# Kernel tuning notes

Measured on AMD Instinct MI355X. Metric: run time of the kernel, lower is better.

The kernel has to match this reference:

```python
import jax, jax.numpy as jnp
import numpy as np
import math

D_MODEL = 512
N_HEADS = 8
D_FF = 2048
EPS = 1e-5

def _layernorm(x, g, b):
    m = jnp.mean(x, axis=-1, keepdims=True)
    v = jnp.var(x, axis=-1, keepdims=True)
    return (x - m) * jax.lax.rsqrt(v + EPS) * g + b

def setup_inputs() -> dict:
    key = jax.random.key(0)
    ks = jax.random.split(key, 8)
    d, dff = D_MODEL, D_FF
    s = lambda fan: 1.0 / math.sqrt(fan)
    return {
        "x": jax.random.normal(ks[0], (4, 2048, d), dtype=jnp.float32),
        "w_qkv": jax.random.normal(ks[1], (d, 3 * d), dtype=jnp.float32) * s(d),
        "b_qkv": jnp.zeros((3 * d,), dtype=jnp.float32),
        "w1": jax.random.normal(ks[2], (d, dff), dtype=jnp.float32) * s(d),
        "b1": jnp.zeros((dff,), dtype=jnp.float32),
        "w2": jax.random.normal(ks[3], (dff, d), dtype=jnp.float32) * s(dff),
        "b2": jnp.zeros((d,), dtype=jnp.float32),
        "g1": jnp.ones((d,), dtype=jnp.float32),
        "be1": jnp.zeros((d,), dtype=jnp.float32),
        "g2": jnp.ones((d,), dtype=jnp.float32),
        "be2": jnp.zeros((d,), dtype=jnp.float32),
    }

def reference(x, w_qkv, b_qkv, w1, b1, w2, b2, g1, be1, g2, be2):
    B, L, d = x.shape
    H = N_HEADS
    hd = d // H
    # Faithful to original: scale = 1/sqrt(hd), scores = qk / scale = qk * sqrt(hd)
    inv_scale = math.sqrt(hd)
    qkv = x @ w_qkv + b_qkv            # [B, L, 3d]
    q, k, v = jnp.split(qkv, 3, axis=-1)
    split_heads = lambda t: t.reshape(B, L, H, hd).transpose(0, 2, 1, 3)  # [B,H,L,hd]
    q, k, v = map(split_heads, (q, k, v))
    scores = jnp.einsum('bhqd,bhkd->bhqk', q, k) * inv_scale
    attn = jax.nn.softmax(scores, axis=-1)
    out = jnp.einsum('bhqk,bhkd->bhqd', attn, v)
    out = out.transpose(0, 2, 1, 3).reshape(B, L, d)
    x = _layernorm(x + out, g1, be1)
    ff = jax.nn.relu(x @ w1 + b1) @ w2 + b2
    return _layernorm(x + ff, g2, be2)
```

## Files before the change

### kernel.cpp

```cpp
#include <hip/hip_runtime.h>

typedef _Float16 f16;
typedef _Float16 f16x4 __attribute__((ext_vector_type(4)));
typedef _Float16 f16x8 __attribute__((ext_vector_type(8)));
typedef float    f32x4 __attribute__((ext_vector_type(4)));

#define QK_SCALE 11.5416528f

__device__ __forceinline__ void g2l16(const void* g, void* l) {
  __builtin_amdgcn_global_load_lds(
      (__attribute__((address_space(1))) const unsigned int*)g,
      (__attribute__((address_space(3))) unsigned int*)l, 16, 0, 0);
}

__device__ __forceinline__ f32x4 mfma16(f16x8 a, f16x8 b, f32x4 c) {
  return __builtin_amdgcn_mfma_f32_16x16x32_f16(a, b, c, 0, 0, 0);
}

__device__ __forceinline__ int swz64(int row, int c) { return row * 64 + ((c ^ (row & 7)) << 3); }
__device__ __forceinline__ int swz32(int row, int c) { return row * 32 + ((c ^ ((row >> 1) & 3)) << 3); }

__global__ __launch_bounds__(256) void k_split(const float* __restrict__ in,
                                               f16* __restrict__ hi, f16* __restrict__ lo, int n4) {
  int i = blockIdx.x * 256 + threadIdx.x;
  if (i >= n4) return;
  f32x4 v = ((const f32x4*)in)[i];
  f16x4 h, l;
#pragma unroll
  for (int j = 0; j < 4; ++j) {
    f16 hv = (f16)v[j];
    h[j] = hv;
    l[j] = (f16)(v[j] - (float)hv);
  }
  ((f16x4*)hi)[i] = h;
  ((f16x4*)lo)[i] = l;
}

template <bool WLO>
__global__ __launch_bounds__(256) void k_transpose_split(const float* __restrict__ in, int K, int N,
                                                         f16* __restrict__ oh, f16* __restrict__ ol) {
  __shared__ float t[32][33];
  const int tx = threadIdx.x, ty = threadIdx.y;
  const int n0 = blockIdx.x * 32, k0 = blockIdx.y * 32;
#pragma unroll
  for (int j = 0; j < 4; ++j)
    t[ty + j * 8][tx] = in[(size_t)(k0 + ty + j * 8) * N + n0 + tx];
  __syncthreads();
#pragma unroll
  for (int j = 0; j < 4; ++j) {
    float v = t[tx][ty + j * 8];
    f16 hv = (f16)v;
    size_t o = (size_t)(n0 + ty + j * 8) * K + k0 + tx;
    oh[o] = hv;
    if (WLO) ol[o] = (f16)(v - (float)hv);
  }
}

template <int EPI, bool SPLIT>
__global__ __launch_bounds__(256, SPLIT ? 2 : 3) void k_gemm(
    const f16* __restrict__ Ah, const f16* __restrict__ Al,
    const f16* __restrict__ Bh, const f16* __restrict__ Bl,
    const float* __restrict__ bias,
    float* __restrict__ outF, f16* __restrict__ outH,
    f16* __restrict__ oqh, f16* __restrict__ oql,
    f16* __restrict__ okh, f16* __restrict__ ovT,
    int M, int N, int K) {
  constexpr int NB = SPLIT ? 2 : 1;
  __shared__ f16 As[NB][128 * 32];
  __shared__ f16 Bs[NB][128 * 32];

  const int tid = threadIdx.x;
  const int bm = blockIdx.x, bn = blockIdx.y;
  const int w = tid >> 6, lane = tid & 63;
  const int wr = w >> 1, wc = w & 1;
  const int lrow = lane & 15, lgrp = lane >> 4;

  f32x4 acc[4][4] = {};

  const int nkt = K >> 5;
  for (int kt = 0; kt < nkt; ++kt) {
    __syncthreads();
    const int kk = kt << 5;
#pragma unroll
    for (int c = 0; c < 2; ++c) {
      const int i = tid + (c << 8);
      const int row = i >> 2;
      const int gch = ((i & 3) ^ ((i >> 3) & 3)) << 3;
      const size_t aoff = (size_t)(bm * 128 + row) * K + kk + gch;
      const size_t boff = (size_t)(bn * 128 + row) * K + kk + gch;
      g2l16(Ah + aoff, &As[0][i * 8]);
      g2l16(Bh + boff, &Bs[0][i * 8]);
      if (SPLIT) {
        g2l16(Al + aoff, &As[1][i * 8]);
        g2l16(Bl + boff, &Bs[1][i * 8]);
      }
    }
    __syncthreads();

    f16x8 a0[4], a1[4], b0[4], b1[4];
#pragma unroll
    for (int mf = 0; mf < 4; ++mf) {
      const int off = swz32(wr * 64 + mf * 16 + lrow, lgrp);
      a0[mf] = *(const f16x8*)&As[0][off];
      if (SPLIT) a1[mf] = *(const f16x8*)&As[SPLIT ? 1 : 0][off];
    }
#pragma unroll
    for (int nf = 0; nf < 4; ++nf) {
      const int off = swz32(wc * 64 + nf * 16 + lrow, lgrp);
      b0[nf] = *(const f16x8*)&Bs[0][off];
      if (SPLIT) b1[nf] = *(const f16x8*)&Bs[SPLIT ? 1 : 0][off];
    }
#pragma unroll
    for (int mf = 0; mf < 4; ++mf)
#pragma unroll
      for (int nf = 0; nf < 4; ++nf) {
        acc[mf][nf] = mfma16(a0[mf], b0[nf], acc[mf][nf]);
        if (SPLIT) {
          acc[mf][nf] = mfma16(a0[mf], b1[nf], acc[mf][nf]);
          acc[mf][nf] = mfma16(a1[mf], b0[nf], acc[mf][nf]);
        }
      }
  }

  const int rowbase = bm * 128 + wr * 64 + lgrp * 4;
  const int colbase = bn * 128 + wc * 64 + lrow;
#pragma unroll
  for (int mf = 0; mf < 4; ++mf) {
#pragma unroll
    for (int nf = 0; nf < 4; ++nf) {
      const int gc = colbase + nf * 16;
      const float bv = bias[gc];
#pragma unroll
      for (int r = 0; r < 4; ++r) {
        const int gr = rowbase + mf * 16 + r;
        const float val = acc[mf][nf][r] + bv;
        if (EPI == 0) {
          const int bb = gr >> 11, tok = gr & 2047;
          const int kind = gc >> 9, hh = (gc >> 6) & 7, dd = gc & 63;
          const size_t bhp = (size_t)((bb << 3) + hh);
          const size_t qidx = (bhp * 2048 + tok) * 64 + dd;
          if (kind == 0) {
            const float sv = val * QK_SCALE;
            const f16 hv = (f16)sv;
            oqh[qidx] = hv; oql[qidx] = (f16)(sv - (float)hv);
          } else if (kind == 1) {
            okh[qidx] = (f16)val;
          } else {
            ovT[(bhp * 64 + dd) * 2048 + tok] = (f16)val;
          }
        } else if (EPI == 1) {
          outH[(size_t)gr * N + gc] = (f16)fmaxf(val, 0.f);
        } else {
          outF[(size_t)gr * N + gc] = val;
        }
      }
    }
  }
}

__global__ __launch_bounds__(256, 3) void k_attn(
    const f16* __restrict__ Qh, const f16* __restrict__ Ql,
    const f16* __restrict__ Kh, const f16* __restrict__ Vt,
    float* __restrict__ out) {
  __shared__ f16 sKh[2][64 * 64], sVt[2][64 * 64];
  __shared__ f16 sPt[4][16 * 64];

  const int tid = threadIdx.x;
  const int qt = blockIdx.x, bh = blockIdx.y;
  const int w = tid >> 6, lane = tid & 63;
  const int lrow = lane & 15, lgrp = lane >> 4;

  const size_t qbase = (((size_t)bh * 2048) + qt * 64 + w * 16) * 64;
  f16x8 qh8[2], ql8[2];
#pragma unroll
  for (int ks = 0; ks < 2; ++ks) {
    const size_t o = qbase + (size_t)lrow * 64 + (ks * 4 + lgrp) * 8;
    qh8[ks] = *(const f16x8*)(Qh + o);
    ql8[ks] = *(const f16x8*)(Ql + o);
  }

  float m_run = -3e38f;
  float l_run = 0.f;
  f32x4 oacc[4] = {};

  auto stage = [&](int b, int kt) {
    const size_t koff = ((size_t)bh * 2048 + (size_t)kt * 64) * 64;
    const size_t voff = (size_t)bh * 64 * 2048 + (size_t)kt * 64;
#pragma unroll
    for (int c = 0; c < 2; ++c) {
      const int i = tid + (c << 8);
      const int row = i >> 3;
      const int gch = ((i & 7) ^ (row & 7)) << 3;
      g2l16(Kh + koff + (size_t)row * 64 + gch, &sKh[b][i * 8]);
      g2l16(Vt + voff + (size_t)row * 2048 + gch, &sVt[b][i * 8]);
    }
  };

  stage(0, 0);
  __syncthreads();

  for (int kt = 0; kt < 32; ++kt) {
    const int cur = kt & 1;
    if (kt < 31) stage(cur ^ 1, kt + 1);

    f32x4 sacc[4] = {};
    __builtin_amdgcn_s_setprio(1);
#pragma unroll
    for (int ks = 0; ks < 2; ++ks) {
#pragma unroll
      for (int kf = 0; kf < 4; ++kf) {
        const int off = swz64(kf * 16 + lrow, ks * 4 + lgrp);
        const f16x8 kh8 = *(const f16x8*)&sKh[cur][off];
        sacc[kf] = mfma16(kh8, qh8[ks], sacc[kf]);
        sacc[kf] = mfma16(kh8, ql8[ks], sacc[kf]);
      }
    }
    __builtin_amdgcn_s_setprio(0);

    {
      float mt = sacc[0][0];
#pragma unroll
      for (int kf = 0; kf < 4; ++kf)
#pragma unroll
        for (int r = 0; r < 4; ++r) mt = fmaxf(mt, sacc[kf][r]);
      mt = fmaxf(mt, __shfl_xor(mt, 16, 64));
      mt = fmaxf(mt, __shfl_xor(mt, 32, 64));
      float mcur = m_run;
      if (!__all(mt <= mcur + 8.0f)) {
        const float mnew = fmaxf(mcur, mt);
        const float corr = __builtin_amdgcn_exp2f(mcur - mnew);
        m_run = mnew;
        l_run *= corr;
#pragma unroll
        for (int hf = 0; hf < 4; ++hf) oacc[hf] = oacc[hf] * corr;
        mcur = mnew;
      }
      float ps = 0.f;
#pragma unroll
      for (int kf = 0; kf < 4; ++kf) {
        f16x4 pv;
#pragma unroll
        for (int r = 0; r < 4; ++r) {
          const float p = __builtin_amdgcn_exp2f(sacc[kf][r] - mcur);
          ps += p;
          pv[r] = (f16)p;
        }
        *(f16x4*)&sPt[w][swz64(lrow, kf * 2 + (lgrp >> 1)) + ((lgrp & 1) << 2)] = pv;
      }
      ps += __shfl_xor(ps, 16, 64);
      ps += __shfl_xor(ps, 32, 64);
      l_run += ps;
    }

    __builtin_amdgcn_s_setprio(1);
#pragma unroll
    for (int ks = 0; ks < 2; ++ks) {
      const f16x8 pb = *(const f16x8*)&sPt[w][swz64(lrow, ks * 4 + lgrp)];
#pragma unroll
      for (int hf = 0; hf < 4; ++hf) {
        const f16x8 va = *(const f16x8*)&sVt[cur][swz64(hf * 16 + lrow, ks * 4 + lgrp)];
        oacc[hf] = mfma16(va, pb, oacc[hf]);
      }
    }
    __builtin_amdgcn_s_setprio(0);
    __syncthreads();
  }

  const int b = bh >> 3, h = bh & 7;
  const float inv = 1.0f / l_run;
  const int t = b * 2048 + qt * 64 + w * 16 + lrow;
#pragma unroll
  for (int hf = 0; hf < 4; ++hf) {
    f32x4 o = oacc[hf] * inv;
    *(f32x4*)(out + (size_t)t * 512 + h * 64 + hf * 16 + lgrp * 4) = o;
  }
}

__global__ __launch_bounds__(64) void k_ln(const float* __restrict__ X, const float* __restrict__ R,
                                           const float* __restrict__ g, const float* __restrict__ be,
                                           float* __restrict__ outF, f16* __restrict__ outH) {
  const int row = blockIdx.x, t = threadIdx.x;
  const size_t base = (size_t)row * 512 + t * 8;
  f32x4 x0 = *(const f32x4*)(X + base);
  f32x4 x1 = *(const f32x4*)(X + base + 4);
  f32x4 r0 = *(const f32x4*)(R + base);
  f32x4 r1 = *(const f32x4*)(R + base + 4);
  x0 = x0 + r0;
  x1 = x1 + r1;
  float s = 0.f, ss = 0.f;
#pragma unroll
  for (int j = 0; j < 4; ++j) { s += x0[j] + x1[j]; ss += x0[j] * x0[j] + x1[j] * x1[j]; }
#pragma unroll
  for (int o = 32; o; o >>= 1) {
    s += __shfl_xor(s, o, 64);
    ss += __shfl_xor(ss, o, 64);
  }
  const float mean = s * (1.f / 512.f);
  const float var = ss * (1.f / 512.f) - mean * mean;
  const float rs = rsqrtf(var + 1e-5f);
  f32x4 g0 = *(const f32x4*)(g + t * 8);
  f32x4 g1v = *(const f32x4*)(g + t * 8 + 4);
  f32x4 b0 = *(const f32x4*)(be + t * 8);
  f32x4 b1 = *(const f32x4*)(be + t * 8 + 4);
  f32x4 y0 = (x0 - mean) * rs * g0 + b0;
  f32x4 y1 = (x1 - mean) * rs * g1v + b1;
  *(f32x4*)(outF + base) = y0;
  *(f32x4*)(outF + base + 4) = y1;
  if (outH != nullptr) {
    f16x8 hx;
#pragma unroll
    for (int j = 0; j < 4; ++j) { hx[j] = (f16)y0[j]; hx[j + 4] = (f16)y1[j]; }
    *(f16x8*)(outH + base) = hx;
  }
}

extern "C" void kernel_launch(void* const* d_in, const int* in_sizes, int n_in,
                              void* d_out, int out_size, void* d_ws, size_t ws_size,
                              hipStream_t stream) {
  (void)in_sizes; (void)n_in; (void)out_size;
  const float* x = (const float*)d_in[0];
  const float* w_qkv = (const float*)d_in[1];
  const float* b_qkv = (const float*)d_in[2];
  const float* w1 = (const float*)d_in[3];
  const float* b1 = (const float*)d_in[4];
  const float* w2 = (const float*)d_in[5];
  const float* b2 = (const float*)d_in[6];
  const float* g1 = (const float*)d_in[7];
  const float* be1 = (const float*)d_in[8];
  const float* g2 = (const float*)d_in[9];
  const float* be2 = (const float*)d_in[10];
  float* out = (float*)d_out;

  char* p = (char*)d_ws;
  auto take = [&](size_t bytes) {
    char* r = p;
    p += (bytes + 255) & ~(size_t)255;
    return r;
  };
  f16* xh = (f16*)take(8192ull * 512 * 2);
  f16* xl = (f16*)take(8192ull * 512 * 2);
  f16* wqkvTh = (f16*)take(1536ull * 512 * 2);
  f16* wqkvTl = (f16*)take(1536ull * 512 * 2);
  f16* w1T = (f16*)take(2048ull * 512 * 2);
  f16* w2T = (f16*)take(512ull * 2048 * 2);
  f16* qh = (f16*)take(32ull * 2048 * 64 * 2);
  f16* ql = (f16*)take(32ull * 2048 * 64 * 2);
  f16* kh = (f16*)take(32ull * 2048 * 64 * 2);
  f16* vT = (f16*)take(32ull * 64 * 2048 * 2);
  float* attn = (float*)take(8192ull * 512 * 4);
  float* x1f = (float*)take(8192ull * 512 * 4);
  f16* x1h = (f16*)take(8192ull * 512 * 2);
  f16* hbuf = qh;
  float* ffb = attn;

  if ((size_t)(p - (char*)d_ws) > ws_size) return;

  dim3 tb(32, 8);
  k_split<<<4096, 256, 0, stream>>>(x, xh, xl, 8192 * 512 / 4);
  k_transpose_split<true><<<dim3(1536 / 32, 512 / 32), tb, 0, stream>>>(w_qkv, 512, 1536, wqkvTh, wqkvTl);
  k_transpose_split<false><<<dim3(2048 / 32, 512 / 32), tb, 0, stream>>>(w1, 512, 2048, w1T, nullptr);
  k_transpose_split<false><<<dim3(512 / 32, 2048 / 32), tb, 0, stream>>>(w2, 2048, 512, w2T, nullptr);

  k_gemm<0, true><<<dim3(64, 12), 256, 0, stream>>>(xh, xl, wqkvTh, wqkvTl, b_qkv,
                                                    nullptr, nullptr, qh, ql, kh, vT,
                                                    8192, 1536, 512);
  k_attn<<<dim3(32, 32), 256, 0, stream>>>(qh, ql, kh, vT, attn);
  k_ln<<<8192, 64, 0, stream>>>(x, attn, g1, be1, x1f, x1h);
  k_gemm<1, false><<<dim3(64, 16), 256, 0, stream>>>(x1h, nullptr, w1T, nullptr, b1,
                                                     nullptr, hbuf, nullptr, nullptr, nullptr, nullptr,
                                                     8192, 2048, 512);
  k_gemm<2, false><<<dim3(64, 4), 256, 0, stream>>>(hbuf, nullptr, w2T, nullptr, b2,
                                                    ffb, nullptr, nullptr, nullptr, nullptr, nullptr,
                                                    8192, 512, 2048);
  k_ln<<<8192, 64, 0, stream>>>(x1f, ffb, g2, be2, out, nullptr);
}
```

Measured before the change: 213.2 us.

## Use 32x32 MFMA in attention with register-resident P and skip lo-split for V

The attention kernel switches from 16x16x32 to 32x32x16 MFMA tiles, with each wave handling 32 query rows and each block 128 rows. The softmax probabilities are packed with cvt_pkrtz and rearranged in registers with permlane32 swaps, so the shared-memory round trip for P is gone. Separately, the QKV GEMM skips the low-part split products for the V columns (bn >= 8), cutting MFMA work and loads there at some cost in V precision. Occupancy drops from 3 to 2 blocks per CU, and there are half as many attention blocks.

```diff
diff --git a/kernel.cpp b/kernel.cpp
--- a/kernel.cpp
+++ b/kernel.cpp
@@ -4,6 +4,8 @@
 typedef _Float16 f16x4 __attribute__((ext_vector_type(4)));
 typedef _Float16 f16x8 __attribute__((ext_vector_type(8)));
 typedef float    f32x4 __attribute__((ext_vector_type(4)));
+typedef float    f32x16 __attribute__((ext_vector_type(16)));
+typedef unsigned int u32x4 __attribute__((ext_vector_type(4)));
 
 #define QK_SCALE 11.5416528f
 
@@ -15,6 +17,16 @@
 
 __device__ __forceinline__ f32x4 mfma16(f16x8 a, f16x8 b, f32x4 c) {
   return __builtin_amdgcn_mfma_f32_16x16x32_f16(a, b, c, 0, 0, 0);
+}
+__device__ __forceinline__ f32x16 mfma32(f16x8 a, f16x8 b, f32x16 c) {
+  return __builtin_amdgcn_mfma_f32_32x32x16_f16(a, b, c, 0, 0, 0);
+}
+__device__ __forceinline__ unsigned pkrtz(float a, float b) {
+  auto t = __builtin_amdgcn_cvt_pkrtz(a, b);
+  return *(unsigned*)&t;
+}
+__device__ __forceinline__ void swap32(unsigned& a, unsigned& b) {
+  asm volatile("v_permlane32_swap_b32 %0, %1" : "+v"(a), "+v"(b));
 }
 
 __device__ __forceinline__ int swz64(int row, int c) { return row * 64 + ((c ^ (row & 7)) << 3); }
@@ -75,6 +87,8 @@
   const int wr = w >> 1, wc = w & 1;
   const int lrow = lane & 15, lgrp = lane >> 4;
 
+  const bool useLo = SPLIT && !(EPI == 0 && bn >= 8);
+
   f32x4 acc[4][4] = {};
 
   const int nkt = K >> 5;
@@ -90,10 +104,11 @@
       const size_t boff = (size_t)(bn * 128 + row) * K + kk + gch;
       g2l16(Ah + aoff, &As[0][i * 8]);
       g2l16(Bh + boff, &Bs[0][i * 8]);
-      if (SPLIT) {
-        g2l16(Al + aoff, &As[1][i * 8]);
-        g2l16(Bl + boff, &Bs[1][i * 8]);
-      }
+      if (SPLIT)
+        if (useLo) {
+          g2l16(Al + aoff, &As[1][i * 8]);
+          g2l16(Bl + boff, &Bs[1][i * 8]);
+        }
     }
     __syncthreads();
 
@@ -102,23 +117,26 @@
     for (int mf = 0; mf < 4; ++mf) {
       const int off = swz32(wr * 64 + mf * 16 + lrow, lgrp);
       a0[mf] = *(const f16x8*)&As[0][off];
-      if (SPLIT) a1[mf] = *(const f16x8*)&As[SPLIT ? 1 : 0][off];
+      if (SPLIT)
+        if (useLo) a1[mf] = *(const f16x8*)&As[SPLIT ? 1 : 0][off];
     }
 #pragma unroll
     for (int nf = 0; nf < 4; ++nf) {
       const int off = swz32(wc * 64 + nf * 16 + lrow, lgrp);
       b0[nf] = *(const f16x8*)&Bs[0][off];
-      if (SPLIT) b1[nf] = *(const f16x8*)&Bs[SPLIT ? 1 : 0][off];
+      if (SPLIT)
+        if (useLo) b1[nf] = *(const f16x8*)&Bs[SPLIT ? 1 : 0][off];
     }
 #pragma unroll
     for (int mf = 0; mf < 4; ++mf)
 #pragma unroll
       for (int nf = 0; nf < 4; ++nf) {
         acc[mf][nf] = mfma16(a0[mf], b0[nf], acc[mf][nf]);
-        if (SPLIT) {
-          acc[mf][nf] = mfma16(a0[mf], b1[nf], acc[mf][nf]);
-          acc[mf][nf] = mfma16(a1[mf], b0[nf], acc[mf][nf]);
-        }
+        if (SPLIT)
+          if (useLo) {
+            acc[mf][nf] = mfma16(a0[mf], b1[nf], acc[mf][nf]);
+            acc[mf][nf] = mfma16(a1[mf], b0[nf], acc[mf][nf]);
+          }
       }
   }
 
@@ -158,30 +176,26 @@
   }
 }
 
-__global__ __launch_bounds__(256, 3) void k_attn(
+__global__ __launch_bounds__(256, 2) void k_attn(
     const f16* __restrict__ Qh, const f16* __restrict__ Ql,
     const f16* __restrict__ Kh, const f16* __restrict__ Vt,
     float* __restrict__ out) {
-  __shared__ f16 sKh[2][64 * 64], sVt[2][64 * 64];
-  __shared__ f16 sPt[4][16 * 64];
+  __shared__ f16 sK[2][64 * 64], sV[2][64 * 64];
 
   const int tid = threadIdx.x;
   const int qt = blockIdx.x, bh = blockIdx.y;
   const int w = tid >> 6, lane = tid & 63;
-  const int lrow = lane & 15, lgrp = lane >> 4;
-
-  const size_t qbase = (((size_t)bh * 2048) + qt * 64 + w * 16) * 64;
-  f16x8 qh8[2], ql8[2];
-#pragma unroll
-  for (int ks = 0; ks < 2; ++ks) {
-    const size_t o = qbase + (size_t)lrow * 64 + (ks * 4 + lgrp) * 8;
-    qh8[ks] = *(const f16x8*)(Qh + o);
-    ql8[ks] = *(const f16x8*)(Ql + o);
-  }
-
-  float m_run = -3e38f;
-  float l_run = 0.f;
-  f32x4 oacc[4] = {};
+  const int lh = lane & 31, hh = lane >> 5;
+
+  const int qrow = qt * 128 + w * 32 + lh;
+  const size_t qoff = ((size_t)bh * 2048 + qrow) * 64;
+  f16x8 qh8[4], ql8[4];
+#pragma unroll
+  for (int d = 0; d < 4; ++d) {
+    const size_t o = qoff + d * 16 + hh * 8;
+    qh8[d] = *(const f16x8*)(Qh + o);
+    ql8[d] = *(const f16x8*)(Ql + o);
+  }
 
   auto stage = [&](int b, int kt) {
     const size_t koff = ((size_t)bh * 2048 + (size_t)kt * 64) * 64;
@@ -191,10 +205,14 @@
       const int i = tid + (c << 8);
       const int row = i >> 3;
       const int gch = ((i & 7) ^ (row & 7)) << 3;
-      g2l16(Kh + koff + (size_t)row * 64 + gch, &sKh[b][i * 8]);
-      g2l16(Vt + voff + (size_t)row * 2048 + gch, &sVt[b][i * 8]);
+      g2l16(Kh + koff + (size_t)row * 64 + gch, &sK[b][i * 8]);
+      g2l16(Vt + voff + (size_t)row * 2048 + gch, &sV[b][i * 8]);
     }
   };
+
+  float m_run = -3e38f;
+  float l_run = 0.f;
+  f32x16 oacc[2] = {};
 
   stage(0, 0);
   __syncthreads();
@@ -203,77 +221,86 @@
     const int cur = kt & 1;
     if (kt < 31) stage(cur ^ 1, kt + 1);
 
-    f32x4 sacc[4] = {};
+    f32x16 s[2] = {};
     __builtin_amdgcn_s_setprio(1);
 #pragma unroll
-    for (int ks = 0; ks < 2; ++ks) {
-#pragma unroll
-      for (int kf = 0; kf < 4; ++kf) {
-        const int off = swz64(kf * 16 + lrow, ks * 4 + lgrp);
-        const f16x8 kh8 = *(const f16x8*)&sKh[cur][off];
-        sacc[kf] = mfma16(kh8, qh8[ks], sacc[kf]);
-        sacc[kf] = mfma16(kh8, ql8[ks], sacc[kf]);
-      }
+    for (int d = 0; d < 4; ++d) {
+      const f16x8 k0 = *(const f16x8*)&sK[cur][swz64(lh, d * 2 + hh)];
+      const f16x8 k1 = *(const f16x8*)&sK[cur][swz64(32 + lh, d * 2 + hh)];
+      s[0] = mfma32(k0, qh8[d], s[0]);
+      s[0] = mfma32(k0, ql8[d], s[0]);
+      s[1] = mfma32(k1, qh8[d], s[1]);
+      s[1] = mfma32(k1, ql8[d], s[1]);
     }
     __builtin_amdgcn_s_setprio(0);
 
-    {
-      float mt = sacc[0][0];
-#pragma unroll
-      for (int kf = 0; kf < 4; ++kf)
-#pragma unroll
-        for (int r = 0; r < 4; ++r) mt = fmaxf(mt, sacc[kf][r]);
-      mt = fmaxf(mt, __shfl_xor(mt, 16, 64));
-      mt = fmaxf(mt, __shfl_xor(mt, 32, 64));
-      float mcur = m_run;
-      if (!__all(mt <= mcur + 8.0f)) {
-        const float mnew = fmaxf(mcur, mt);
-        const float corr = __builtin_amdgcn_exp2f(mcur - mnew);
-        m_run = mnew;
-        l_run *= corr;
-#pragma unroll
-        for (int hf = 0; hf < 4; ++hf) oacc[hf] = oacc[hf] * corr;
-        mcur = mnew;
-      }
-      float ps = 0.f;
-#pragma unroll
-      for (int kf = 0; kf < 4; ++kf) {
-        f16x4 pv;
-#pragma unroll
-        for (int r = 0; r < 4; ++r) {
-          const float p = __builtin_amdgcn_exp2f(sacc[kf][r] - mcur);
-          ps += p;
-          pv[r] = (f16)p;
-        }
-        *(f16x4*)&sPt[w][swz64(lrow, kf * 2 + (lgrp >> 1)) + ((lgrp & 1) << 2)] = pv;
-      }
-      ps += __shfl_xor(ps, 16, 64);
-      ps += __shfl_xor(ps, 32, 64);
-      l_run += ps;
-    }
+    float mt = s[0][0];
+#pragma unroll
+    for (int r = 0; r < 16; ++r) { mt = fmaxf(mt, s[0][r]); mt = fmaxf(mt, s[1][r]); }
+    mt = fmaxf(mt, __shfl_xor(mt, 32, 64));
+    float mcur = m_run;
+    if (!__all(mt <= mcur + 8.0f)) {
+      const float mnew = fmaxf(mcur, mt);
+      const float corr = __builtin_amdgcn_exp2f(mcur - mnew);
+      m_run = mnew;
+      l_run *= corr;
+      oacc[0] = oacc[0] * corr;
+      oacc[1] = oacc[1] * corr;
+      mcur = mnew;
+    }
+    float ps = 0.f;
+    unsigned pk0[8], pk1[8];
+#pragma unroll
+    for (int i = 0; i < 8; ++i) {
+      const float a0 = __builtin_amdgcn_exp2f(s[0][2 * i] - mcur);
+      const float a1 = __builtin_amdgcn_exp2f(s[0][2 * i + 1] - mcur);
+      const float b0 = __builtin_amdgcn_exp2f(s[1][2 * i] - mcur);
+      const float b1 = __builtin_amdgcn_exp2f(s[1][2 * i + 1] - mcur);
+      ps += (a0 + a1) + (b0 + b1);
+      pk0[i] = pkrtz(a0, a1);
+      pk1[i] = pkrtz(b0, b1);
+    }
+    ps += __shfl_xor(ps, 32, 64);
+    l_run += ps;
+
+    swap32(pk0[0], pk0[2]); swap32(pk0[1], pk0[3]);
+    swap32(pk0[4], pk0[6]); swap32(pk0[5], pk0[7]);
+    swap32(pk1[0], pk1[2]); swap32(pk1[1], pk1[3]);
+    swap32(pk1[4], pk1[6]); swap32(pk1[5], pk1[7]);
+
+    u32x4 pbu[4];
+    pbu[0] = (u32x4){pk0[0], pk0[1], pk0[2], pk0[3]};
+    pbu[1] = (u32x4){pk0[4], pk0[5], pk0[6], pk0[7]};
+    pbu[2] = (u32x4){pk1[0], pk1[1], pk1[2], pk1[3]};
+    pbu[3] = (u32x4){pk1[4], pk1[5], pk1[6], pk1[7]};
 
     __builtin_amdgcn_s_setprio(1);
 #pragma unroll
-    for (int ks = 0; ks < 2; ++ks) {
-      const f16x8 pb = *(const f16x8*)&sPt[w][swz64(lrow, ks * 4 + lgrp)];
-#pragma unroll
-      for (int hf = 0; hf < 4; ++hf) {
-        const f16x8 va = *(const f16x8*)&sVt[cur][swz64(hf * 16 + lrow, ks * 4 + lgrp)];
-        oacc[hf] = mfma16(va, pb, oacc[hf]);
+    for (int s2 = 0; s2 < 4; ++s2) {
+      const f16x8 pb = *(const f16x8*)&pbu[s2];
+#pragma unroll
+      for (int db = 0; db < 2; ++db) {
+        const f16x8 v = *(const f16x8*)&sV[cur][swz64(db * 32 + lh, s2 * 2 + hh)];
+        oacc[db] = mfma32(v, pb, oacc[db]);
       }
     }
     __builtin_amdgcn_s_setprio(0);
     __syncthreads();
   }
 
-  const int b = bh >> 3, h = bh & 7;
+  const int b = bh >> 3, hd = bh & 7;
   const float inv = 1.0f / l_run;
-  const int t = b * 2048 + qt * 64 + w * 16 + lrow;
-#pragma unroll
-  for (int hf = 0; hf < 4; ++hf) {
-    f32x4 o = oacc[hf] * inv;
-    *(f32x4*)(out + (size_t)t * 512 + h * 64 + hf * 16 + lgrp * 4) = o;
-  }
+  const int trow = b * 2048 + qt * 128 + w * 32 + lh;
+  float* po = out + (size_t)trow * 512 + hd * 64;
+#pragma unroll
+  for (int db = 0; db < 2; ++db)
+#pragma unroll
+    for (int rq = 0; rq < 4; ++rq) {
+      f32x4 o;
+#pragma unroll
+      for (int j = 0; j < 4; ++j) o[j] = oacc[db][rq * 4 + j] * inv;
+      *(f32x4*)(po + db * 32 + rq * 8 + hh * 4) = o;
+    }
 }
 
 __global__ __launch_bounds__(64) void k_ln(const float* __restrict__ X, const float* __restrict__ R,
@@ -364,7 +391,7 @@
   k_gemm<0, true><<<dim3(64, 12), 256, 0, stream>>>(xh, xl, wqkvTh, wqkvTl, b_qkv,
                                                     nullptr, nullptr, qh, ql, kh, vT,
                                                     8192, 1536, 512);
-  k_attn<<<dim3(32, 32), 256, 0, stream>>>(qh, ql, kh, vT, attn);
+  k_attn<<<dim3(16, 32), 256, 0, stream>>>(qh, ql, kh, vT, attn);
   k_ln<<<8192, 64, 0, stream>>>(x, attn, g1, be1, x1f, x1h);
   k_gemm<1, false><<<dim3(64, 16), 256, 0, stream>>>(x1h, nullptr, w1T, nullptr, b1,
                                                      nullptr, hbuf, nullptr, nullptr, nullptr, nullptr,
```

Result: faster. 204.3 us (-4.2%).
